# Kernel tuning notes

Measured on AMD Instinct MI355X. Metric: run time of the kernel, lower is better.

The kernel has to match this reference:

```python
import jax, jax.numpy as jnp
import numpy as np

B, S, H = 2, 1024, 2048
NH, NKV, HD = 16, 8, 128
GROUPS = NH // NKV
THETA = 1000000.0
SPARSITY = 0.4  # q_len > 512 -> vision_sparse_attention_sparsity_ratio
TOP_K = max(1, min(S, int(SPARSITY * S)))


def _rope(q, k, position_ids):
    # inv_freq: [HD/2]
    inv_freq = 1.0 / (THETA ** (jnp.arange(0, HD, 2, dtype=jnp.float32) / HD))
    freqs = position_ids.astype(jnp.float32)[:, :, None] * inv_freq  # [B,S,HD/2]
    emb = jnp.concatenate([freqs, freqs], axis=-1)                   # [B,S,HD]
    cos = jnp.cos(emb)[:, None].astype(q.dtype)  # [B,1,S,HD] (unsqueeze_dim=1)
    sin = jnp.sin(emb)[:, None].astype(q.dtype)
    rot = lambda x: jnp.concatenate([-x[..., HD // 2:], x[..., :HD // 2]], axis=-1)
    return q * cos + rot(q) * sin, k * cos + rot(k) * sin


def setup_inputs() -> dict:
    key = jax.random.key(0)
    ks = jax.random.split(key, 10)
    sc = 0.02
    inp = {
        'hidden_states': jax.random.normal(ks[0], (B, S, H), jnp.float32),
        'wq': jax.random.normal(ks[1], (NH * HD, H), jnp.float32) * sc,
        'bq': jax.random.normal(ks[2], (NH * HD,), jnp.float32) * sc,
        'wk': jax.random.normal(ks[3], (NKV * HD, H), jnp.float32) * sc,
        'bk': jax.random.normal(ks[4], (NKV * HD,), jnp.float32) * sc,
        'wv': jax.random.normal(ks[5], (NKV * HD, H), jnp.float32) * sc,
        'bv': jax.random.normal(ks[6], (NKV * HD,), jnp.float32) * sc,
        'wo': jax.random.normal(ks[7], (H, NH * HD), jnp.float32) * sc,
        'bo': jax.random.normal(ks[8], (H,), jnp.float32) * sc,
        'position_ids': jnp.tile(jnp.arange(S, dtype=jnp.int32)[None, :], (B, 1)),
    }
    return inp


def reference(hidden_states, wq, bq, wk, bk, wv, bv, wo, bo, position_ids):
    # QKV projections -> [B, heads, S, HD]
    q = (hidden_states @ wq.T + bq).reshape(B, S, NH, HD).transpose(0, 2, 1, 3)
    k = (hidden_states @ wk.T + bk).reshape(B, S, NKV, HD).transpose(0, 2, 1, 3)
    v = (hidden_states @ wv.T + bv).reshape(B, S, NKV, HD).transpose(0, 2, 1, 3)

    q, k = _rope(q, k, position_ids)

    # GQA: repeat_interleave KV heads along head axis
    k = jnp.repeat(k, GROUPS, axis=1)
    v = jnp.repeat(v, GROUPS, axis=1)

    scores = jnp.einsum('bhqd,bhkd->bhqk', q, k) / jnp.sqrt(jnp.float32(HD))

    # VectorizedSparseAttention: keep top-k weights per query, -inf elsewhere
    topk_vals = jax.lax.top_k(scores, TOP_K)[0]          # sorted descending
    thresh = topk_vals[..., -1:]                         # k-th largest per row
    sparse = jnp.where(scores >= thresh, scores, -jnp.inf)

    probs = jax.nn.softmax(sparse.astype(jnp.float32), axis=-1).astype(q.dtype)
    attn = jnp.einsum('bhqk,bhkd->bhqd', probs, v)       # [B,NH,S,HD]
    attn = attn.transpose(0, 2, 1, 3).reshape(B, S, NH * HD)
    return attn @ wo.T + bo
```

## Files before the change

### kernel.cpp

```cpp
#include <hip/hip_runtime.h>
#include <hip/hip_bf16.h>

constexpr int B_ = 2, S_ = 1024, H_ = 2048;
constexpr int NH_ = 16, NKV_ = 8, HD_ = 128, GROUPS_ = 2;
constexpr int TOPK_ = 409;
constexpr int QSTRIDE = NH_ * HD_;
constexpr int KSTRIDE = NKV_ * HD_;
constexpr int QB_ = 16;

typedef __attribute__((ext_vector_type(8))) short short8;
typedef __attribute__((ext_vector_type(4))) float f32x4;
typedef __attribute__((ext_vector_type(4))) unsigned u32x4;

__device__ inline unsigned fkey(float x) {
  unsigned u = __float_as_uint(x);
  return (u & 0x80000000u) ? ~u : (u | 0x80000000u);
}
__device__ inline unsigned short bf16_rne(float x) {
  unsigned u = __float_as_uint(x);
  unsigned r = u + 0x7FFFu + ((u >> 16) & 1u);
  return (unsigned short)(r >> 16);
}
__device__ inline float bf16_to_f(unsigned short h) {
  return __uint_as_float((unsigned)h << 16);
}
__device__ inline unsigned packsplit(float x) {
  unsigned u = __float_as_uint(x);
  unsigned r = (u + 0x7FFFu + ((u >> 16) & 1u)) & 0xFFFF0000u;
  float rem = x - __uint_as_float(r);
  unsigned v = __float_as_uint(rem);
  unsigned l = (v + 0x7FFFu + ((v >> 16) & 1u)) >> 16;
  return r | l;
}

#define PERM_HI 0x07060302u
#define PERM_LO 0x05040100u

__device__ inline void unpack8(const unsigned* p, short8& hi, short8& lo) {
  u32x4 w0 = *(const u32x4*)p;
  u32x4 w1 = *(const u32x4*)(p + 4);
  u32x4 h, l;
  h.x = __builtin_amdgcn_perm(w0.y, w0.x, PERM_HI);
  h.y = __builtin_amdgcn_perm(w0.w, w0.z, PERM_HI);
  h.z = __builtin_amdgcn_perm(w1.y, w1.x, PERM_HI);
  h.w = __builtin_amdgcn_perm(w1.w, w1.z, PERM_HI);
  l.x = __builtin_amdgcn_perm(w0.y, w0.x, PERM_LO);
  l.y = __builtin_amdgcn_perm(w0.w, w0.z, PERM_LO);
  l.z = __builtin_amdgcn_perm(w1.y, w1.x, PERM_LO);
  l.w = __builtin_amdgcn_perm(w1.w, w1.z, PERM_LO);
  hi = *(short8*)&h;
  lo = *(short8*)&l;
}

__device__ inline void wave_lds_fence() {
  asm volatile("s_waitcnt lgkmcnt(0)" ::: "memory");
}

template <int TI>
__device__ __forceinline__ void gemm_split_body(
    const float* __restrict__ A, const float* __restrict__ W,
    const float* __restrict__ bias, float* __restrict__ C, int ldc, int c0,
    int K, int m0) {
  __shared__ unsigned short Ah[TI * 32][32];
  __shared__ unsigned short Al[TI * 32][32];
  __shared__ unsigned short Wh[128][32];
  __shared__ unsigned short Wl[128][32];
  const int tid = threadIdx.x;
  const int lane = tid & 63, wid = tid >> 6;
  const int wrow = (wid >> 1) * (TI * 16), wcol = (wid & 1) * 64;
  const int fm = lane & 15, quad = lane >> 4;
  const int srow = tid >> 3;
  const int skq = (tid & 7) * 4;
  f32x4 acc[TI][4] = {};

  for (int k0 = 0; k0 < K; k0 += 32) {
    __syncthreads();
#pragma unroll
    for (int r = 0; r < TI; ++r) {
      int row = srow + 32 * r;
      float4 av = *(const float4*)&A[(size_t)(m0 + row) * K + k0 + skq];
      unsigned short h0 = bf16_rne(av.x), h1 = bf16_rne(av.y),
                     h2 = bf16_rne(av.z), h3 = bf16_rne(av.w);
      Ah[row][skq + 0] = h0; Ah[row][skq + 1] = h1;
      Ah[row][skq + 2] = h2; Ah[row][skq + 3] = h3;
      Al[row][skq + 0] = bf16_rne(av.x - bf16_to_f(h0));
      Al[row][skq + 1] = bf16_rne(av.y - bf16_to_f(h1));
      Al[row][skq + 2] = bf16_rne(av.z - bf16_to_f(h2));
      Al[row][skq + 3] = bf16_rne(av.w - bf16_to_f(h3));
    }
#pragma unroll
    for (int r = 0; r < 4; ++r) {
      int row = srow + 32 * r;
      float4 wv2 = *(const float4*)&W[(size_t)row * K + k0 + skq];
      unsigned short g0 = bf16_rne(wv2.x), g1 = bf16_rne(wv2.y),
                     g2 = bf16_rne(wv2.z), g3 = bf16_rne(wv2.w);
      Wh[row][skq + 0] = g0; Wh[row][skq + 1] = g1;
      Wh[row][skq + 2] = g2; Wh[row][skq + 3] = g3;
      Wl[row][skq + 0] = bf16_rne(wv2.x - bf16_to_f(g0));
      Wl[row][skq + 1] = bf16_rne(wv2.y - bf16_to_f(g1));
      Wl[row][skq + 2] = bf16_rne(wv2.z - bf16_to_f(g2));
      Wl[row][skq + 3] = bf16_rne(wv2.w - bf16_to_f(g3));
    }
    __syncthreads();
    short8 ah[TI], al[TI], bh[4], bl[4];
#pragma unroll
    for (int ti = 0; ti < TI; ++ti) {
      ah[ti] = *(const short8*)&Ah[wrow + 16 * ti + fm][quad * 8];
      al[ti] = *(const short8*)&Al[wrow + 16 * ti + fm][quad * 8];
    }
#pragma unroll
    for (int tj = 0; tj < 4; ++tj) {
      bh[tj] = *(const short8*)&Wh[wcol + 16 * tj + fm][quad * 8];
      bl[tj] = *(const short8*)&Wl[wcol + 16 * tj + fm][quad * 8];
    }
#pragma unroll
    for (int ti = 0; ti < TI; ++ti)
#pragma unroll
      for (int tj = 0; tj < 4; ++tj) {
        acc[ti][tj] = __builtin_amdgcn_mfma_f32_16x16x32_bf16(
            ah[ti], bh[tj], acc[ti][tj], 0, 0, 0);
        acc[ti][tj] = __builtin_amdgcn_mfma_f32_16x16x32_bf16(
            ah[ti], bl[tj], acc[ti][tj], 0, 0, 0);
        acc[ti][tj] = __builtin_amdgcn_mfma_f32_16x16x32_bf16(
            al[ti], bh[tj], acc[ti][tj], 0, 0, 0);
      }
  }
#pragma unroll
  for (int tj = 0; tj < 4; ++tj) {
    float bsv = bias[wcol + 16 * tj + fm];
#pragma unroll
    for (int ti = 0; ti < TI; ++ti) {
      int mrow = m0 + wrow + 16 * ti + quad * 4;
      int ncol = c0 + wcol + 16 * tj + fm;
#pragma unroll
      for (int reg = 0; reg < 4; ++reg)
        C[(size_t)(mrow + reg) * ldc + ncol] = acc[ti][tj][reg] + bsv;
    }
  }
}

__global__ __launch_bounds__(256) void gemm_qkv(
    const float* __restrict__ hidden, const float* __restrict__ wq,
    const float* __restrict__ bq, const float* __restrict__ wk,
    const float* __restrict__ bk, const float* __restrict__ wv,
    const float* __restrict__ bv, float* __restrict__ q, float* __restrict__ k,
    float* __restrict__ v) {
  const int n0 = blockIdx.x * 128, m0 = blockIdx.y * 128;
  const float* W;
  const float* bias;
  float* C;
  int ldc, c0;
  if (n0 < QSTRIDE) {
    W = wq + (size_t)n0 * H_; bias = bq + n0; C = q; ldc = QSTRIDE; c0 = n0;
  } else if (n0 < QSTRIDE + KSTRIDE) {
    int nn = n0 - QSTRIDE;
    W = wk + (size_t)nn * H_; bias = bk + nn; C = k; ldc = KSTRIDE; c0 = nn;
  } else {
    int nn = n0 - QSTRIDE - KSTRIDE;
    W = wv + (size_t)nn * H_; bias = bv + nn; C = v; ldc = KSTRIDE; c0 = nn;
  }
  gemm_split_body<4>(hidden, W, bias, C, ldc, c0, H_, m0);
}

template <int TI>
__global__ __launch_bounds__(256) void gemm_split_k(
    const float* __restrict__ A, const float* __restrict__ W,
    const float* __restrict__ bias, float* __restrict__ C, int N, int K) {
  const int n0 = blockIdx.x * 128, m0 = blockIdx.y * (TI * 32);
  gemm_split_body<TI>(A, W + (size_t)n0 * K, bias + n0, C, N, n0, K, m0);
}

__global__ __launch_bounds__(64) void rope_pack(float* __restrict__ qtmp,
                                                float* __restrict__ ktmp,
                                                float* __restrict__ vtmp,
                                                const int* __restrict__ pos_ids) {
  const int s = blockIdx.x, hh = blockIdx.y, b = blockIdx.z;
  const int d = threadIdx.x;
  if (hh >= NH_ + NKV_) {
    float* ptr = vtmp + (size_t)(b * S_ + s) * KSTRIDE + (hh - NH_ - NKV_) * HD_;
    float x = ptr[d], y = ptr[d + 64];
    unsigned* up = (unsigned*)ptr;
    up[d] = packsplit(x);
    up[d + 64] = packsplit(y);
    return;
  }
  const int pos = pos_ids[b * S_ + s];
  float* ptr = (hh < NH_)
                   ? qtmp + (size_t)(b * S_ + s) * QSTRIDE + hh * HD_
                   : ktmp + (size_t)(b * S_ + s) * KSTRIDE + (hh - NH_) * HD_;
  float x = ptr[d], y = ptr[d + 64];
  float f = (float)(1.0 / pow(1.0e6, (double)d / 64.0));
  float ang = (float)pos * f;
  float c = cosf(ang), sn = sinf(ang);
  unsigned* up = (unsigned*)ptr;
  up[d] = packsplit(x * c - y * sn);
  up[d + 64] = packsplit(y * c + x * sn);
}

constexpr int SCW = 1028;
constexpr int KVP = 132;

__global__ __launch_bounds__(512, 1) void attn_kernel(
    unsigned* __restrict__ qpk, const unsigned* __restrict__ kpk,
    const unsigned* __restrict__ vpk) {
  const int q0 = blockIdx.x * QB_;
  const int h = blockIdx.y, b = blockIdx.z, g = h / GROUPS_;
  const int t = threadIdx.x, lane = t & 63, wid = t >> 6;
  const int fm = lane & 15, quad = lane >> 4;

  __shared__ float sc[QB_ * SCW];
  __shared__ unsigned kvt[128 * KVP];
  __shared__ unsigned qst[QB_][KVP];
  __shared__ unsigned hist[8][256];
  __shared__ float redmx[8][QB_];
  __shared__ float Zsh[QB_];
  __shared__ unsigned prefix_sh[QB_];
  __shared__ unsigned selbin_sh[8];
  __shared__ int selkk_sh[8];
  const float scale = 0.08838834764831845f;

  const int kt = t >> 5;
  const int st = (t & 31) * 4;
  const int stsw = st ^ (((kt >> 3) & 1) << 4);

  {
    int qi = t >> 5, c4 = (t & 31) * 4;
    u32x4 v = *(const u32x4*)&qpk[(size_t)(b * S_ + q0 + qi) * QSTRIDE +
                                  h * HD_ + c4];
    *(u32x4*)&qst[qi][c4] = v;
  }
  const unsigned* kg = kpk + (size_t)(b * S_) * KSTRIDE + g * HD_;
  u32x4 pf[8];
#pragma unroll
  for (int j = 0; j < 8; ++j)
    pf[j] = *(const u32x4*)&kg[(size_t)(kt + 16 * j) * KSTRIDE + st];
  __syncthreads();

  short8 qh[4], ql[4];
#pragma unroll
  for (int ks = 0; ks < 4; ++ks)
    unpack8(&qst[fm][ks * 32 + quad * 8], qh[ks], ql[ks]);

  const int kswz = ((fm >> 3) & 1) << 4;
  f32x4 mxacc = {-1e30f, -1e30f, -1e30f, -1e30f};
  for (int tile = 0; tile < 8; ++tile) {
    if (tile) __syncthreads();
#pragma unroll
    for (int j = 0; j < 8; ++j)
      *(u32x4*)&kvt[(kt + 16 * j) * KVP + stsw] = pf[j];
    __syncthreads();
    if (tile < 7) {
#pragma unroll
      for (int j = 0; j < 8; ++j)
        pf[j] = *(const u32x4*)&kg[(size_t)((tile + 1) * 128 + kt + 16 * j) *
                                       KSTRIDE + st];
    }
    f32x4 acc = {0.f, 0.f, 0.f, 0.f};
    const int krow = wid * 16 + fm;
#pragma unroll
    for (int ks = 0; ks < 4; ++ks) {
      short8 bh, bl;
      unpack8(&kvt[krow * KVP + ((ks * 32 + quad * 8) ^ kswz)], bh, bl);
      acc = __builtin_amdgcn_mfma_f32_16x16x32_bf16(qh[ks], bh, acc, 0, 0, 0);
      acc = __builtin_amdgcn_mfma_f32_16x16x32_bf16(qh[ks], bl, acc, 0, 0, 0);
      acc = __builtin_amdgcn_mfma_f32_16x16x32_bf16(ql[ks], bh, acc, 0, 0, 0);
    }
    const int key = tile * 128 + krow;
#pragma unroll
    for (int reg = 0; reg < 4; ++reg) {
      float sval = acc[reg] * scale;
      sc[(quad * 4 + reg) * SCW + key] = sval;
      mxacc[reg] = fmaxf(mxacc[reg], sval);
    }
  }
#pragma unroll
  for (int o = 1; o < 16; o <<= 1) {
    mxacc[0] = fmaxf(mxacc[0], __shfl_xor(mxacc[0], o));
    mxacc[1] = fmaxf(mxacc[1], __shfl_xor(mxacc[1], o));
    mxacc[2] = fmaxf(mxacc[2], __shfl_xor(mxacc[2], o));
    mxacc[3] = fmaxf(mxacc[3], __shfl_xor(mxacc[3], o));
  }
  if (fm == 0) {
#pragma unroll
    for (int reg = 0; reg < 4; ++reg) redmx[wid][quad * 4 + reg] = mxacc[reg];
  }
  __syncthreads();

  const unsigned* vg = vpk + (size_t)(b * S_) * KSTRIDE + g * HD_;
  u32x4 vf[8];
#pragma unroll
  for (int j = 0; j < 8; ++j)
    vf[j] = *(const u32x4*)&vg[(size_t)(kt + 16 * j) * KSTRIDE + st];

  for (int sq = 0; sq < 2; ++sq) {
    const int qi = wid * 2 + sq;
    int kk = TOPK_;
    unsigned prefix = 0;
    for (int pass = 0; pass < 4; ++pass) {
      const int shift = 24 - 8 * pass;
      const unsigned pmask = pass ? (0xFFFFFFFFu << (shift + 8)) : 0u;
      *(u32x4*)&hist[wid][4 * lane] = (u32x4){0, 0, 0, 0};
      wave_lds_fence();
#pragma unroll 4
      for (int j = 0; j < 16; ++j) {
        unsigned u = fkey(sc[qi * SCW + lane + 64 * j]);
        if ((u & pmask) == (prefix & pmask))
          atomicAdd(&hist[wid][(u >> shift) & 255], 1u);
      }
      wave_lds_fence();
      u32x4 cw = *(const u32x4*)&hist[wid][4 * lane];
      int c0 = (int)cw.x, c1 = (int)cw.y, c2 = (int)cw.z, c3 = (int)cw.w;
      int s3 = c3, s2 = c2 + s3, s1 = c1 + s2, s0 = c0 + s1;
      int tot = s0;
      int suf = tot;
#pragma unroll
      for (int off = 1; off < 64; off <<= 1) {
        int vv = __shfl_down(suf, off);
        if (lane + off < 64) suf += vv;
      }
      int above_lanes = suf - tot;
      int i0 = s0 + above_lanes, i1 = s1 + above_lanes;
      int i2 = s2 + above_lanes, i3 = s3 + above_lanes;
      if (i3 >= kk && i3 - c3 < kk) {
        selbin_sh[wid] = (unsigned)(4 * lane + 3); selkk_sh[wid] = kk - (i3 - c3);
      }
      if (i2 >= kk && i2 - c2 < kk) {
        selbin_sh[wid] = (unsigned)(4 * lane + 2); selkk_sh[wid] = kk - (i2 - c2);
      }
      if (i1 >= kk && i1 - c1 < kk) {
        selbin_sh[wid] = (unsigned)(4 * lane + 1); selkk_sh[wid] = kk - (i1 - c1);
      }
      if (i0 >= kk && i0 - c0 < kk) {
        selbin_sh[wid] = (unsigned)(4 * lane + 0); selkk_sh[wid] = kk - (i0 - c0);
      }
      wave_lds_fence();
      prefix |= selbin_sh[wid] << shift;
      kk = selkk_sh[wid];
    }
    if (lane == 0) prefix_sh[qi] = prefix;
  }
  wave_lds_fence();

  {
    const int qi = t >> 5, li = t & 31;
    const float mx =
        fmaxf(fmaxf(fmaxf(redmx[0][qi], redmx[1][qi]),
                    fmaxf(redmx[2][qi], redmx[3][qi])),
              fmaxf(fmaxf(redmx[4][qi], redmx[5][qi]),
                    fmaxf(redmx[6][qi], redmx[7][qi])));
    const unsigned pref = prefix_sh[qi];
    unsigned* scp = (unsigned*)&sc[qi * SCW];
    float zloc = 0.f;
#pragma unroll 2
    for (int j = 0; j < 8; ++j) {
      int i4 = li * 4 + 128 * j;
      f32x4 sv = *(const f32x4*)&sc[qi * SCW + i4];
      u32x4 pk;
      float p0 = (fkey(sv.x) >= pref) ? __expf(sv.x - mx) : 0.0f;
      float p1 = (fkey(sv.y) >= pref) ? __expf(sv.y - mx) : 0.0f;
      float p2 = (fkey(sv.z) >= pref) ? __expf(sv.z - mx) : 0.0f;
      float p3 = (fkey(sv.w) >= pref) ? __expf(sv.w - mx) : 0.0f;
      zloc += p0 + p1 + p2 + p3;
      pk.x = packsplit(p0); pk.y = packsplit(p1);
      pk.z = packsplit(p2); pk.w = packsplit(p3);
      *(u32x4*)&scp[i4] = pk;
    }
#pragma unroll
    for (int off = 1; off < 32; off <<= 1) zloc += __shfl_xor(zloc, off);
    if (li == 0) Zsh[qi] = zloc;
  }

  const unsigned* scp2 = (const unsigned*)sc;
  f32x4 oacc = {0.f, 0.f, 0.f, 0.f};
  const int dim = wid * 16 + fm;
  for (int tile = 0; tile < 8; ++tile) {
    __syncthreads();
#pragma unroll
    for (int j = 0; j < 8; ++j)
      *(u32x4*)&kvt[(kt + 16 * j) * KVP + stsw] = vf[j];
    __syncthreads();
    if (tile < 7) {
#pragma unroll
      for (int j = 0; j < 8; ++j)
        vf[j] = *(const u32x4*)&vg[(size_t)((tile + 1) * 128 + kt + 16 * j) *
                                       KSTRIDE + st];
    }
    const int dsw = dim ^ ((quad & 1) << 4);
#pragma unroll
    for (int ks = 0; ks < 4; ++ks) {
      short8 ph, pl;
      unpack8(&scp2[fm * SCW + tile * 128 + ks * 32 + quad * 8], ph, pl);
      const int rb = ks * 32 + quad * 8;
      unsigned w0 = kvt[(rb + 0) * KVP + dsw];
      unsigned w1 = kvt[(rb + 1) * KVP + dsw];
      unsigned w2 = kvt[(rb + 2) * KVP + dsw];
      unsigned w3 = kvt[(rb + 3) * KVP + dsw];
      unsigned w4 = kvt[(rb + 4) * KVP + dsw];
      unsigned w5 = kvt[(rb + 5) * KVP + dsw];
      unsigned w6 = kvt[(rb + 6) * KVP + dsw];
      unsigned w7 = kvt[(rb + 7) * KVP + dsw];
      u32x4 hq, lq;
      hq.x = __builtin_amdgcn_perm(w1, w0, PERM_HI);
      hq.y = __builtin_amdgcn_perm(w3, w2, PERM_HI);
      hq.z = __builtin_amdgcn_perm(w5, w4, PERM_HI);
      hq.w = __builtin_amdgcn_perm(w7, w6, PERM_HI);
      lq.x = __builtin_amdgcn_perm(w1, w0, PERM_LO);
      lq.y = __builtin_amdgcn_perm(w3, w2, PERM_LO);
      lq.z = __builtin_amdgcn_perm(w5, w4, PERM_LO);
      lq.w = __builtin_amdgcn_perm(w7, w6, PERM_LO);
      short8 vh = *(short8*)&hq;
      short8 vl = *(short8*)&lq;
      oacc = __builtin_amdgcn_mfma_f32_16x16x32_bf16(ph, vh, oacc, 0, 0, 0);
      oacc = __builtin_amdgcn_mfma_f32_16x16x32_bf16(ph, vl, oacc, 0, 0, 0);
      oacc = __builtin_amdgcn_mfma_f32_16x16x32_bf16(pl, vh, oacc, 0, 0, 0);
    }
  }

#pragma unroll
  for (int reg = 0; reg < 4; ++reg) {
    const int q = quad * 4 + reg;
    const float invZ = 1.0f / Zsh[q];
    float* outp = (float*)qpk + (size_t)(b * S_ + q0 + q) * QSTRIDE + h * HD_;
    outp[dim] = oacc[reg] * invZ;
  }
}

extern "C" void kernel_launch(void* const* d_in, const int* in_sizes, int n_in,
                              void* d_out, int out_size, void* d_ws,
                              size_t ws_size, hipStream_t stream) {
  const float* hidden = (const float*)d_in[0];
  const float* wq = (const float*)d_in[1];
  const float* bq = (const float*)d_in[2];
  const float* wk = (const float*)d_in[3];
  const float* bk = (const float*)d_in[4];
  const float* wv = (const float*)d_in[5];
  const float* bv = (const float*)d_in[6];
  const float* wo = (const float*)d_in[7];
  const float* bo = (const float*)d_in[8];
  const int* pos = (const int*)d_in[9];
  float* out = (float*)d_out;

  char* ws = (char*)d_ws;
  float* qtmp = (float*)ws;
  float* ktmp = (float*)(ws + ((size_t)16 << 20));
  float* vtmp = (float*)(ws + ((size_t)24 << 20));

  dim3 blk(256);
  gemm_qkv<<<dim3(32, 16), blk, 0, stream>>>(hidden, wq, bq, wk, bk, wv, bv,
                                             qtmp, ktmp, vtmp);
  rope_pack<<<dim3(S_, NH_ + 2 * NKV_, B_), dim3(64), 0, stream>>>(qtmp, ktmp,
                                                                   vtmp, pos);
  attn_kernel<<<dim3(S_ / QB_, NH_, B_), dim3(512), 0, stream>>>(
      (unsigned*)qtmp, (const unsigned*)ktmp, (const unsigned*)vtmp);
  gemm_split_k<2><<<dim3(H_ / 128, (B_ * S_) / 64), blk, 0, stream>>>(
      qtmp, wo, bo, out, H_, H_);
}
```

Baseline: 636.5 us.

## Double-buffer split-bf16 GEMM tiles with swizzled LDS and batch RoPE per token

```diff
diff --git a/kernel.cpp b/kernel.cpp
--- a/kernel.cpp
+++ b/kernel.cpp
@@ -11,6 +11,7 @@
 typedef __attribute__((ext_vector_type(8))) short short8;
 typedef __attribute__((ext_vector_type(4))) float f32x4;
 typedef __attribute__((ext_vector_type(4))) unsigned u32x4;
+typedef __attribute__((ext_vector_type(4))) unsigned short ush4;
 
 __device__ inline unsigned fkey(float x) {
   unsigned u = __float_as_uint(x);
@@ -61,10 +62,10 @@
     const float* __restrict__ A, const float* __restrict__ W,
     const float* __restrict__ bias, float* __restrict__ C, int ldc, int c0,
     int K, int m0) {
-  __shared__ unsigned short Ah[TI * 32][32];
-  __shared__ unsigned short Al[TI * 32][32];
-  __shared__ unsigned short Wh[128][32];
-  __shared__ unsigned short Wl[128][32];
+  __shared__ unsigned short Ah[2][TI * 32 * 32];
+  __shared__ unsigned short Al[2][TI * 32 * 32];
+  __shared__ unsigned short Wh[2][128 * 32];
+  __shared__ unsigned short Wl[2][128 * 32];
   const int tid = threadIdx.x;
   const int lane = tid & 63, wid = tid >> 6;
   const int wrow = (wid >> 1) * (TI * 16), wcol = (wid & 1) * 64;
@@ -72,46 +73,72 @@
   const int srow = tid >> 3;
   const int skq = (tid & 7) * 4;
   f32x4 acc[TI][4] = {};
-
+  float4 avr[TI], wvr[4];
+
+  auto loadAW = [&](int k0) {
+#pragma unroll
+    for (int r = 0; r < TI; ++r)
+      avr[r] = *(const float4*)&A[(size_t)(m0 + srow + 32 * r) * K + k0 + skq];
+#pragma unroll
+    for (int r = 0; r < 4; ++r)
+      wvr[r] = *(const float4*)&W[(size_t)(srow + 32 * r) * K + k0 + skq];
+  };
+  auto convWrite = [&](int buf) {
+#pragma unroll
+    for (int r = 0; r < TI; ++r) {
+      const int row = srow + 32 * r;
+      const int off =
+          row * 32 + ((((skq >> 3) ^ ((row >> 1) & 3)) << 3) | (skq & 7));
+      unsigned short h0 = bf16_rne(avr[r].x), h1 = bf16_rne(avr[r].y),
+                     h2 = bf16_rne(avr[r].z), h3 = bf16_rne(avr[r].w);
+      ush4 hv; hv.x = h0; hv.y = h1; hv.z = h2; hv.w = h3;
+      ush4 lv;
+      lv.x = bf16_rne(avr[r].x - bf16_to_f(h0));
+      lv.y = bf16_rne(avr[r].y - bf16_to_f(h1));
+      lv.z = bf16_rne(avr[r].z - bf16_to_f(h2));
+      lv.w = bf16_rne(avr[r].w - bf16_to_f(h3));
+      *(ush4*)&Ah[buf][off] = hv;
+      *(ush4*)&Al[buf][off] = lv;
+    }
+#pragma unroll
+    for (int r = 0; r < 4; ++r) {
+      const int row = srow + 32 * r;
+      const int off =
+          row * 32 + ((((skq >> 3) ^ ((row >> 1) & 3)) << 3) | (skq & 7));
+      unsigned short g0 = bf16_rne(wvr[r].x), g1 = bf16_rne(wvr[r].y),
+                     g2 = bf16_rne(wvr[r].z), g3 = bf16_rne(wvr[r].w);
+      ush4 hv; hv.x = g0; hv.y = g1; hv.z = g2; hv.w = g3;
+      ush4 lv;
+      lv.x = bf16_rne(wvr[r].x - bf16_to_f(g0));
+      lv.y = bf16_rne(wvr[r].y - bf16_to_f(g1));
+      lv.z = bf16_rne(wvr[r].z - bf16_to_f(g2));
+      lv.w = bf16_rne(wvr[r].w - bf16_to_f(g3));
+      *(ush4*)&Wh[buf][off] = hv;
+      *(ush4*)&Wl[buf][off] = lv;
+    }
+  };
+
+  loadAW(0);
+  convWrite(0);
+  __syncthreads();
+  int cur = 0;
   for (int k0 = 0; k0 < K; k0 += 32) {
-    __syncthreads();
-#pragma unroll
-    for (int r = 0; r < TI; ++r) {
-      int row = srow + 32 * r;
-      float4 av = *(const float4*)&A[(size_t)(m0 + row) * K + k0 + skq];
-      unsigned short h0 = bf16_rne(av.x), h1 = bf16_rne(av.y),
-                     h2 = bf16_rne(av.z), h3 = bf16_rne(av.w);
-      Ah[row][skq + 0] = h0; Ah[row][skq + 1] = h1;
-      Ah[row][skq + 2] = h2; Ah[row][skq + 3] = h3;
-      Al[row][skq + 0] = bf16_rne(av.x - bf16_to_f(h0));
-      Al[row][skq + 1] = bf16_rne(av.y - bf16_to_f(h1));
-      Al[row][skq + 2] = bf16_rne(av.z - bf16_to_f(h2));
-      Al[row][skq + 3] = bf16_rne(av.w - bf16_to_f(h3));
-    }
-#pragma unroll
-    for (int r = 0; r < 4; ++r) {
-      int row = srow + 32 * r;
-      float4 wv2 = *(const float4*)&W[(size_t)row * K + k0 + skq];
-      unsigned short g0 = bf16_rne(wv2.x), g1 = bf16_rne(wv2.y),
-                     g2 = bf16_rne(wv2.z), g3 = bf16_rne(wv2.w);
-      Wh[row][skq + 0] = g0; Wh[row][skq + 1] = g1;
-      Wh[row][skq + 2] = g2; Wh[row][skq + 3] = g3;
-      Wl[row][skq + 0] = bf16_rne(wv2.x - bf16_to_f(g0));
-      Wl[row][skq + 1] = bf16_rne(wv2.y - bf16_to_f(g1));
-      Wl[row][skq + 2] = bf16_rne(wv2.z - bf16_to_f(g2));
-      Wl[row][skq + 3] = bf16_rne(wv2.w - bf16_to_f(g3));
-    }
-    __syncthreads();
+    const bool more = (k0 + 32) < K;
+    if (more) loadAW(k0 + 32);
     short8 ah[TI], al[TI], bh[4], bl[4];
 #pragma unroll
     for (int ti = 0; ti < TI; ++ti) {
-      ah[ti] = *(const short8*)&Ah[wrow + 16 * ti + fm][quad * 8];
-      al[ti] = *(const short8*)&Al[wrow + 16 * ti + fm][quad * 8];
+      const int r = wrow + 16 * ti + fm;
+      const int off = r * 32 + ((quad ^ ((r >> 1) & 3)) << 3);
+      ah[ti] = *(const short8*)&Ah[cur][off];
+      al[ti] = *(const short8*)&Al[cur][off];
     }
 #pragma unroll
     for (int tj = 0; tj < 4; ++tj) {
-      bh[tj] = *(const short8*)&Wh[wcol + 16 * tj + fm][quad * 8];
-      bl[tj] = *(const short8*)&Wl[wcol + 16 * tj + fm][quad * 8];
+      const int r = wcol + 16 * tj + fm;
+      const int off = r * 32 + ((quad ^ ((r >> 1) & 3)) << 3);
+      bh[tj] = *(const short8*)&Wh[cur][off];
+      bl[tj] = *(const short8*)&Wl[cur][off];
     }
 #pragma unroll
     for (int ti = 0; ti < TI; ++ti)
@@ -124,6 +151,9 @@
         acc[ti][tj] = __builtin_amdgcn_mfma_f32_16x16x32_bf16(
             al[ti], bh[tj], acc[ti][tj], 0, 0, 0);
       }
+    if (more) convWrite(cur ^ 1);
+    __syncthreads();
+    cur ^= 1;
   }
 #pragma unroll
   for (int tj = 0; tj < 4; ++tj) {
@@ -170,31 +200,40 @@
   gemm_split_body<TI>(A, W + (size_t)n0 * K, bias + n0, C, N, n0, K, m0);
 }
 
-__global__ __launch_bounds__(64) void rope_pack(float* __restrict__ qtmp,
-                                                float* __restrict__ ktmp,
-                                                float* __restrict__ vtmp,
-                                                const int* __restrict__ pos_ids) {
-  const int s = blockIdx.x, hh = blockIdx.y, b = blockIdx.z;
-  const int d = threadIdx.x;
-  if (hh >= NH_ + NKV_) {
-    float* ptr = vtmp + (size_t)(b * S_ + s) * KSTRIDE + (hh - NH_ - NKV_) * HD_;
-    float x = ptr[d], y = ptr[d + 64];
-    unsigned* up = (unsigned*)ptr;
-    up[d] = packsplit(x);
-    up[d + 64] = packsplit(y);
-    return;
-  }
+__global__ __launch_bounds__(256) void rope_pack(float* __restrict__ qtmp,
+                                                 float* __restrict__ ktmp,
+                                                 float* __restrict__ vtmp,
+                                                 const int* __restrict__ pos_ids) {
+  const int s = blockIdx.x, b = blockIdx.y;
+  const int t = threadIdx.x;
+  __shared__ float fsh[64];
+  if (t < 64) fsh[t] = (float)(1.0 / pow(1.0e6, (double)t / 64.0));
+  __syncthreads();
   const int pos = pos_ids[b * S_ + s];
-  float* ptr = (hh < NH_)
-                   ? qtmp + (size_t)(b * S_ + s) * QSTRIDE + hh * HD_
-                   : ktmp + (size_t)(b * S_ + s) * KSTRIDE + (hh - NH_) * HD_;
-  float x = ptr[d], y = ptr[d + 64];
-  float f = (float)(1.0 / pow(1.0e6, (double)d / 64.0));
-  float ang = (float)pos * f;
-  float c = cosf(ang), sn = sinf(ang);
-  unsigned* up = (unsigned*)ptr;
-  up[d] = packsplit(x * c - y * sn);
-  up[d + 64] = packsplit(y * c + x * sn);
+#pragma unroll
+  for (int it = 0; it < 8; ++it) {
+    const int p = t + 256 * it;
+    const int slot = p >> 6;
+    const int d = p & 63;
+    float* base;
+    if (slot < NH_)
+      base = qtmp + (size_t)(b * S_ + s) * QSTRIDE + slot * HD_;
+    else if (slot < NH_ + NKV_)
+      base = ktmp + (size_t)(b * S_ + s) * KSTRIDE + (slot - NH_) * HD_;
+    else
+      base = vtmp + (size_t)(b * S_ + s) * KSTRIDE + (slot - NH_ - NKV_) * HD_;
+    float x = base[d], y = base[d + 64];
+    unsigned* up = (unsigned*)base;
+    if (slot < NH_ + NKV_) {
+      float ang = (float)pos * fsh[d];
+      float c = cosf(ang), sn = sinf(ang);
+      up[d] = packsplit(x * c - y * sn);
+      up[d + 64] = packsplit(y * c + x * sn);
+    } else {
+      up[d] = packsplit(x);
+      up[d + 64] = packsplit(y);
+    }
+  }
 }
 
 constexpr int SCW = 1028;
@@ -448,8 +487,7 @@
   dim3 blk(256);
   gemm_qkv<<<dim3(32, 16), blk, 0, stream>>>(hidden, wq, bq, wk, bk, wv, bv,
                                              qtmp, ktmp, vtmp);
-  rope_pack<<<dim3(S_, NH_ + 2 * NKV_, B_), dim3(64), 0, stream>>>(qtmp, ktmp,
-                                                                   vtmp, pos);
+  rope_pack<<<dim3(S_, B_), dim3(256), 0, stream>>>(qtmp, ktmp, vtmp, pos);
   attn_kernel<<<dim3(S_ / QB_, NH_, B_), dim3(512), 0, stream>>>(
       (unsigned*)qtmp, (const unsigned*)ktmp, (const unsigned*)vtmp);
   gemm_split_k<2><<<dim3(H_ / 128, (B_ * S_) / 64), blk, 0, stream>>>(
```

Result: faster. 598.9 us (-5.9%).
